# Kernel tuning notes

Hardware: AMD Instinct MI355X
Metric: run time of the kernel (lower is better)

The kernel has to match this reference:

```python
import jax, jax.numpy as jnp
import numpy as np

N_NODES = 50000
HIDDEN = 128
N_EDGES = 1_600_000


def gcn_conv(x, W, b, src, dst, n_nodes):
    """PyG GCNConv: linear, add self-loops, symmetric deg^-1/2 normalization, scatter-sum."""
    h = x @ W  # [N, D]
    # degree with self-loops: 1 + in-degree from edges (edge weight 1)
    deg = jnp.ones((n_nodes,), h.dtype).at[dst].add(1.0)
    dinv = jax.lax.rsqrt(deg)  # deg^{-1/2}, deg >= 1 so no inf
    # neighbor messages: norm_e = dinv[src] * dinv[dst]
    msgs = h[src] * (dinv[src] * dinv[dst])[:, None]  # [E, D]
    agg = jnp.zeros_like(h).at[dst].add(msgs)
    # self-loop contribution: norm = dinv[i]*dinv[i]
    agg = agg + h * (dinv * dinv)[:, None]
    return agg + b


def setup_inputs() -> dict:
    key = jax.random.key(0)
    ks = jax.random.split(key, 7)
    x = jax.random.normal(ks[0], (N_NODES, HIDDEN), dtype=jnp.float32)
    edge_index = jax.random.randint(ks[1], (2, N_EDGES), 0, N_NODES, dtype=jnp.int64)
    s = 1.0 / np.sqrt(HIDDEN)
    W1 = jax.random.uniform(ks[2], (HIDDEN, HIDDEN), jnp.float32, -s, s)
    b1 = jax.random.uniform(ks[3], (HIDDEN,), jnp.float32, -s, s)
    W2 = jax.random.uniform(ks[4], (HIDDEN, HIDDEN), jnp.float32, -s, s)
    b2 = jax.random.uniform(ks[5], (HIDDEN,), jnp.float32, -s, s)
    return {"x": x, "edge_index": edge_index, "W1": W1, "b1": b1, "W2": W2, "b2": b2}


def reference(x, edge_index, W1, b1, W2, b2):
    src, dst = edge_index[0], edge_index[1]
    h = jax.nn.relu(gcn_conv(x, W1, b1, src, dst, N_NODES))
    z = gcn_conv(h, W2, b2, src, dst, N_NODES)
    return z
```

## Files before the change

### kernel.cpp

```cpp
#include <hip/hip_runtime.h>
#include <hip/hip_fp16.h>
#include <type_traits>

#define D 128


__global__ __launch_bounds__(256) void deg_kernel(const int* __restrict__ dst,
                                                  int* __restrict__ deg,
                                                  int* __restrict__ rank, int E) {
  int e = blockIdx.x * 256 + threadIdx.x;
  if (e < E) rank[e] = atomicAdd(&deg[dst[e]], 1);
}


__global__ __launch_bounds__(256) void bsum_kernel(const int* __restrict__ deg,
                                                   int* __restrict__ bsum) {
  __shared__ int ws[4];
  int i0 = blockIdx.x * 1024 + threadIdx.x * 4;
  int4 v = *reinterpret_cast<const int4*>(deg + i0);
  int s = v.x + v.y + v.z + v.w;
  #pragma unroll
  for (int off = 32; off; off >>= 1) s += __shfl_down(s, off);
  if ((threadIdx.x & 63) == 0) ws[threadIdx.x >> 6] = s;
  __syncthreads();
  if (threadIdx.x == 0) bsum[blockIdx.x] = ws[0] + ws[1] + ws[2] + ws[3];
}


__global__ __launch_bounds__(256) void scan_kernel(const int* __restrict__ deg,
                                                   const int* __restrict__ bsum,
                                                   int* __restrict__ offsets,
                                                   float* __restrict__ dinv,
                                                   int N, int E) {
  __shared__ int ts[256];
  int b = blockIdx.x;
  int base = 0;
  for (int t = 0; t < b; ++t) base += bsum[t];

  int i0 = b * 1024 + threadIdx.x * 4;
  int4 v = *reinterpret_cast<const int4*>(deg + i0);
  int t4 = v.x + v.y + v.z + v.w;
  ts[threadIdx.x] = t4;
  __syncthreads();
  #pragma unroll
  for (int off = 1; off < 256; off <<= 1) {
    int u = (threadIdx.x >= off) ? ts[threadIdx.x - off] : 0;
    __syncthreads();
    ts[threadIdx.x] += u;
    __syncthreads();
  }
  int run = base + ts[threadIdx.x] - t4;

  int dd[4] = {v.x, v.y, v.z, v.w};
  #pragma unroll
  for (int k = 0; k < 4; ++k) {
    int i = i0 + k;
    if (i < N) {
      offsets[i] = run;
      dinv[i] = rsqrtf(1.0f + (float)dd[k]);
    }
    run += dd[k];
  }
  if (b == 0 && threadIdx.x == 0) offsets[N] = E;
}


__global__ __launch_bounds__(256) void place_kernel(const int* __restrict__ src,
                                                    const int* __restrict__ dst,
                                                    const int* __restrict__ rank,
                                                    const int* __restrict__ offsets,
                                                    const float* __restrict__ dinv,
                                                    unsigned int* __restrict__ csr, int E) {
  int t = blockIdx.x * 256 + threadIdx.x;
  int e0 = t * 4;
  if (e0 + 4 <= E) {
    int4 s4 = *reinterpret_cast<const int4*>(src + e0);
    int4 d4 = *reinterpret_cast<const int4*>(dst + e0);
    int4 r4 = *reinterpret_cast<const int4*>(rank + e0);
    int ss[4] = {s4.x, s4.y, s4.z, s4.w};
    int dd[4] = {d4.x, d4.y, d4.z, d4.w};
    int rr[4] = {r4.x, r4.y, r4.z, r4.w};
    int pos[4];
    float nm[4];
    #pragma unroll
    for (int k = 0; k < 4; ++k) pos[k] = offsets[dd[k]] + rr[k];
    #pragma unroll
    for (int k = 0; k < 4; ++k) nm[k] = dinv[ss[k]] * dinv[dd[k]];
    #pragma unroll
    for (int k = 0; k < 4; ++k) {
      unsigned int q = (unsigned int)__float2int_rn(nm[k] * 32767.0f);
      csr[pos[k]] = ((unsigned int)ss[k] << 15) | q;
    }
  } else {
    for (int e = e0; e < E; ++e) {
      int s = src[e];
      int d = dst[e];
      int pos = offsets[d] + rank[e];
      float nm = dinv[s] * dinv[d];
      unsigned int q = (unsigned int)__float2int_rn(nm * 32767.0f);
      csr[pos] = ((unsigned int)s << 15) | q;
    }
  }
}


template <typename TI>
__global__ __launch_bounds__(256) void gemm_kernel(const TI* __restrict__ X,
                                                   const float* __restrict__ W,
                                                   __half* __restrict__ H, int N) {
  __shared__ float xs[32 * D];
  int row0 = blockIdx.x * 32;
  if constexpr (std::is_same<TI, float>::value) {
    #pragma unroll
    for (int jj = 0; jj < 4; ++jj) {
      int f4 = threadIdx.x + jj * 256;
      int r = f4 >> 5;
      float4 v = make_float4(0.f, 0.f, 0.f, 0.f);
      if (row0 + r < N) v = *reinterpret_cast<const float4*>(X + (size_t)row0 * D + (size_t)f4 * 4);
      *reinterpret_cast<float4*>(xs + f4 * 4) = v;
    }
  } else {
    #pragma unroll
    for (int jj = 0; jj < 2; ++jj) {
      int g8 = threadIdx.x + jj * 256;
      int r = g8 >> 4;
      uint4 raw = make_uint4(0u, 0u, 0u, 0u);
      if (row0 + r < N)
        raw = *reinterpret_cast<const uint4*>((const __half*)X + (size_t)row0 * D + (size_t)g8 * 8);
      const __half2* hp = reinterpret_cast<const __half2*>(&raw);
      float* dst8 = xs + (size_t)g8 * 8;
      #pragma unroll
      for (int k = 0; k < 4; ++k) {
        float2 f = __half22float2(hp[k]);
        dst8[k * 2] = f.x;
        dst8[k * 2 + 1] = f.y;
      }
    }
  }
  __syncthreads();

  int tx = threadIdx.x & 63;
  int ty = threadIdx.x >> 6;
  int c0 = tx * 2;
  float2 acc[8];
  #pragma unroll
  for (int r = 0; r < 8; ++r) acc[r] = make_float2(0.f, 0.f);
  const float* xbase = xs + ty * 8 * D;

  for (int k = 0; k < D; k += 4) {
    float2 w0 = *reinterpret_cast<const float2*>(W + (size_t)(k + 0) * D + c0);
    float2 w1 = *reinterpret_cast<const float2*>(W + (size_t)(k + 1) * D + c0);
    float2 w2 = *reinterpret_cast<const float2*>(W + (size_t)(k + 2) * D + c0);
    float2 w3 = *reinterpret_cast<const float2*>(W + (size_t)(k + 3) * D + c0);
    #pragma unroll
    for (int r = 0; r < 8; ++r) {
      float4 xv = *reinterpret_cast<const float4*>(xbase + r * D + k);
      acc[r].x = fmaf(xv.x, w0.x, acc[r].x); acc[r].y = fmaf(xv.x, w0.y, acc[r].y);
      acc[r].x = fmaf(xv.y, w1.x, acc[r].x); acc[r].y = fmaf(xv.y, w1.y, acc[r].y);
      acc[r].x = fmaf(xv.z, w2.x, acc[r].x); acc[r].y = fmaf(xv.z, w2.y, acc[r].y);
      acc[r].x = fmaf(xv.w, w3.x, acc[r].x); acc[r].y = fmaf(xv.w, w3.y, acc[r].y);
    }
  }

  #pragma unroll
  for (int r = 0; r < 8; ++r) {
    int row = row0 + ty * 8 + r;
    if (row < N)
      *reinterpret_cast<__half2*>(H + (size_t)row * D + c0) = __floats2half2_rn(acc[r].x, acc[r].y);
  }
}


template <int DO_RELU, typename TO>
__global__ __launch_bounds__(256) void agg_kernel(const __half* __restrict__ H,
                                                  const int* __restrict__ offsets,
                                                  const unsigned int* __restrict__ csr,
                                                  const float* __restrict__ dinv,
                                                  const float* __restrict__ bias,
                                                  TO* __restrict__ out, int N) {
  int n = blockIdx.x * 4 + (threadIdx.x >> 6);
  if (n >= N) return;
  int lane = threadIdx.x & 63;
  int g = lane >> 4;
  int l = lane & 15;

  int beg = offsets[n];
  int end = offsets[n + 1];

  float acc[8];
  #pragma unroll
  for (int k = 0; k < 8; ++k) acc[k] = 0.f;

  const __half* Hl = H + l * 8;

  int j = beg + g;
  for (; j + 12 < end; j += 16) {
    unsigned int p0 = csr[j];
    unsigned int p1 = csr[j + 4];
    unsigned int p2 = csr[j + 8];
    unsigned int p3 = csr[j + 12];
    float m0 = (float)(p0 & 0x7fffu) * (1.0f / 32767.0f);
    float m1 = (float)(p1 & 0x7fffu) * (1.0f / 32767.0f);
    float m2 = (float)(p2 & 0x7fffu) * (1.0f / 32767.0f);
    float m3 = (float)(p3 & 0x7fffu) * (1.0f / 32767.0f);
    uint4 r0 = *reinterpret_cast<const uint4*>(Hl + (size_t)(p0 >> 15) * D);
    uint4 r1 = *reinterpret_cast<const uint4*>(Hl + (size_t)(p1 >> 15) * D);
    uint4 r2 = *reinterpret_cast<const uint4*>(Hl + (size_t)(p2 >> 15) * D);
    uint4 r3 = *reinterpret_cast<const uint4*>(Hl + (size_t)(p3 >> 15) * D);
    const __half2* h0 = reinterpret_cast<const __half2*>(&r0);
    const __half2* h1 = reinterpret_cast<const __half2*>(&r1);
    const __half2* h2 = reinterpret_cast<const __half2*>(&r2);
    const __half2* h3 = reinterpret_cast<const __half2*>(&r3);
    #pragma unroll
    for (int k = 0; k < 4; ++k) {
      float2 f0 = __half22float2(h0[k]);
      float2 f1 = __half22float2(h1[k]);
      float2 f2 = __half22float2(h2[k]);
      float2 f3 = __half22float2(h3[k]);
      acc[2 * k]     = fmaf(f0.x, m0, acc[2 * k]);
      acc[2 * k + 1] = fmaf(f0.y, m0, acc[2 * k + 1]);
      acc[2 * k]     = fmaf(f1.x, m1, acc[2 * k]);
      acc[2 * k + 1] = fmaf(f1.y, m1, acc[2 * k + 1]);
      acc[2 * k]     = fmaf(f2.x, m2, acc[2 * k]);
      acc[2 * k + 1] = fmaf(f2.y, m2, acc[2 * k + 1]);
      acc[2 * k]     = fmaf(f3.x, m3, acc[2 * k]);
      acc[2 * k + 1] = fmaf(f3.y, m3, acc[2 * k + 1]);
    }
  }
  for (; j < end; j += 4) {
    unsigned int p0 = csr[j];
    float m0 = (float)(p0 & 0x7fffu) * (1.0f / 32767.0f);
    uint4 r0 = *reinterpret_cast<const uint4*>(Hl + (size_t)(p0 >> 15) * D);
    const __half2* h0 = reinterpret_cast<const __half2*>(&r0);
    #pragma unroll
    for (int k = 0; k < 4; ++k) {
      float2 f0 = __half22float2(h0[k]);
      acc[2 * k]     = fmaf(f0.x, m0, acc[2 * k]);
      acc[2 * k + 1] = fmaf(f0.y, m0, acc[2 * k + 1]);
    }
  }

  #pragma unroll
  for (int k = 0; k < 8; ++k) {
    acc[k] += __shfl_xor(acc[k], 16);
    acc[k] += __shfl_xor(acc[k], 32);
  }

  if (g == 0) {
    float di = dinv[n];
    float dii = di * di;
    uint4 rs = *reinterpret_cast<const uint4*>(Hl + (size_t)n * D);
    const __half2* hs = reinterpret_cast<const __half2*>(&rs);
    float4 bv0 = *reinterpret_cast<const float4*>(bias + l * 8);
    float4 bv1 = *reinterpret_cast<const float4*>(bias + l * 8 + 4);
    float v[8];
    #pragma unroll
    for (int k = 0; k < 4; ++k) {
      float2 f = __half22float2(hs[k]);
      v[2 * k]     = fmaf(f.x, dii, acc[2 * k]);
      v[2 * k + 1] = fmaf(f.y, dii, acc[2 * k + 1]);
    }
    v[0] += bv0.x; v[1] += bv0.y; v[2] += bv0.z; v[3] += bv0.w;
    v[4] += bv1.x; v[5] += bv1.y; v[6] += bv1.z; v[7] += bv1.w;
    if (DO_RELU) {
      #pragma unroll
      for (int k = 0; k < 8; ++k) v[k] = fmaxf(v[k], 0.f);
    }
    if constexpr (std::is_same<TO, float>::value) {
      float4 o0 = make_float4(v[0], v[1], v[2], v[3]);
      float4 o1 = make_float4(v[4], v[5], v[6], v[7]);
      *reinterpret_cast<float4*>(out + (size_t)n * D + l * 8) = o0;
      *reinterpret_cast<float4*>(out + (size_t)n * D + l * 8 + 4) = o1;
    } else {
      uint4 pk;
      __half2 q0 = __floats2half2_rn(v[0], v[1]);
      __half2 q1 = __floats2half2_rn(v[2], v[3]);
      __half2 q2 = __floats2half2_rn(v[4], v[5]);
      __half2 q3 = __floats2half2_rn(v[6], v[7]);
      pk.x = *reinterpret_cast<unsigned int*>(&q0);
      pk.y = *reinterpret_cast<unsigned int*>(&q1);
      pk.z = *reinterpret_cast<unsigned int*>(&q2);
      pk.w = *reinterpret_cast<unsigned int*>(&q3);
      *reinterpret_cast<uint4*>((__half*)out + (size_t)n * D + l * 8) = pk;
    }
  }
}


extern "C" void kernel_launch(void* const* d_in, const int* in_sizes, int n_in,
                              void* d_out, int out_size, void* d_ws, size_t ws_size,
                              hipStream_t stream) {
  const float* x  = (const float*)d_in[0];
  const int* edge = (const int*)d_in[1];
  const float* W1 = (const float*)d_in[2];
  const float* b1 = (const float*)d_in[3];
  const float* W2 = (const float*)d_in[4];
  const float* b2 = (const float*)d_in[5];
  const int N = in_sizes[0] / D;
  const int E = in_sizes[1] / 2;
  const int* srcp = edge;
  const int* dstp = edge + E;
  float* out = (float*)d_out;

  const int NP = (N + 1023) & ~1023;
  const int SB = NP / 1024;

  auto align = [](size_t v) { return (v + 255) & ~(size_t)255; };
  char* ws = (char*)d_ws;
  size_t o = 0;
  int*   deg     = (int*)(ws + o);             o += align((size_t)NP * 4);
  int*   bsum    = (int*)(ws + o);             o += align((size_t)SB * 4);
  int*   offsets = (int*)(ws + o);             o += align((size_t)(N + 1) * 4);
  int*   rank    = (int*)(ws + o);             o += align((size_t)E * 4);
  float* dinv    = (float*)(ws + o);           o += align((size_t)N * 4);
  unsigned int* csr = (unsigned int*)(ws + o); o += align((size_t)E * 4);
  __half* Hh     = (__half*)(ws + o);          o += align((size_t)N * D * 2);
  __half* h1h    = (__half*)(ws + o);          o += align((size_t)N * D * 2);

  int gemm_blocks = (N + 31) / 32;
  int agg_blocks  = (N + 3) / 4;

  hipMemsetAsync(deg, 0, (size_t)NP * 4, stream);
  deg_kernel<<<(E + 255) / 256, 256, 0, stream>>>(dstp, deg, rank, E);
  bsum_kernel<<<SB, 256, 0, stream>>>(deg, bsum);
  scan_kernel<<<SB, 256, 0, stream>>>(deg, bsum, offsets, dinv, N, E);
  int pl_threads = (E + 3) / 4;
  place_kernel<<<(pl_threads + 255) / 256, 256, 0, stream>>>(srcp, dstp, rank, offsets, dinv, csr, E);

  gemm_kernel<float><<<gemm_blocks, 256, 0, stream>>>(x, W1, Hh, N);
  agg_kernel<1, __half><<<agg_blocks, 256, 0, stream>>>(Hh, offsets, csr, dinv, b1, h1h, N);

  gemm_kernel<__half><<<gemm_blocks, 256, 0, stream>>>(h1h, W2, Hh, N);
  agg_kernel<0, float><<<agg_blocks, 256, 0, stream>>>(Hh, offsets, csr, dinv, b2, out, N);
}
```

Before: 281.3 us.

## Build CSR via per-chunk shared-memory histograms instead of global atomics

Replaces the global atomicAdd degree/rank pass with a two-level counting sort. Edge chunks are histogrammed in LDS per node range, a column-wise prefix over chunks gives per-chunk offsets, and placement uses LDS atomics to assign slots. This removes contended global atomics and the rank array, at the cost of a 128×N count matrix (about 25 MB of extra traffic), re-reading dst once per node-range block, and non-deterministic ordering within chunks.

```diff
diff --git a/kernel.cpp b/kernel.cpp
--- a/kernel.cpp
+++ b/kernel.cpp
@@ -3,13 +3,43 @@
 #include <type_traits>
 
 #define D 128
-
-
-__global__ __launch_bounds__(256) void deg_kernel(const int* __restrict__ dst,
-                                                  int* __restrict__ deg,
-                                                  int* __restrict__ rank, int E) {
-  int e = blockIdx.x * 256 + threadIdx.x;
-  if (e < E) rank[e] = atomicAdd(&deg[dst[e]], 1);
+#define NI 128
+#define NR 25000
+
+
+__global__ __launch_bounds__(1024) void histA_kernel(const int* __restrict__ dst,
+                                                     int* __restrict__ c,
+                                                     int E, int N, int CH) {
+  __shared__ int cnt[NR];
+  int i = blockIdx.x, r = blockIdx.y;
+  int base = r * NR;
+  int kmax = min(NR, N - base);
+  for (int k = threadIdx.x; k < kmax; k += 1024) cnt[k] = 0;
+  __syncthreads();
+  int e0 = i * CH, e1 = min(e0 + CH, E);
+  for (int e = e0 + (int)threadIdx.x; e < e1; e += 1024) {
+    unsigned dr = (unsigned)(dst[e] - base);
+    if (dr < (unsigned)kmax) atomicAdd(&cnt[dr], 1);
+  }
+  __syncthreads();
+  int* ci = c + (size_t)i * N + base;
+  for (int k = threadIdx.x; k < kmax; k += 1024) ci[k] = cnt[k];
+}
+
+
+__global__ __launch_bounds__(256) void histB_kernel(int* __restrict__ c,
+                                                    int* __restrict__ deg, int N) {
+  int n = blockIdx.x * 256 + threadIdx.x;
+  if (n >= N) return;
+  int run = 0;
+  #pragma unroll 8
+  for (int i = 0; i < NI; ++i) {
+    size_t idx = (size_t)i * N + n;
+    int v = c[idx];
+    c[idx] = run;
+    run += v;
+  }
+  deg[n] = run;
 }
 
 
@@ -65,37 +95,27 @@
 }
 
 
-__global__ __launch_bounds__(256) void place_kernel(const int* __restrict__ src,
-                                                    const int* __restrict__ dst,
-                                                    const int* __restrict__ rank,
-                                                    const int* __restrict__ offsets,
-                                                    const float* __restrict__ dinv,
-                                                    unsigned int* __restrict__ csr, int E) {
-  int t = blockIdx.x * 256 + threadIdx.x;
-  int e0 = t * 4;
-  if (e0 + 4 <= E) {
-    int4 s4 = *reinterpret_cast<const int4*>(src + e0);
-    int4 d4 = *reinterpret_cast<const int4*>(dst + e0);
-    int4 r4 = *reinterpret_cast<const int4*>(rank + e0);
-    int ss[4] = {s4.x, s4.y, s4.z, s4.w};
-    int dd[4] = {d4.x, d4.y, d4.z, d4.w};
-    int rr[4] = {r4.x, r4.y, r4.z, r4.w};
-    int pos[4];
-    float nm[4];
-    #pragma unroll
-    for (int k = 0; k < 4; ++k) pos[k] = offsets[dd[k]] + rr[k];
-    #pragma unroll
-    for (int k = 0; k < 4; ++k) nm[k] = dinv[ss[k]] * dinv[dd[k]];
-    #pragma unroll
-    for (int k = 0; k < 4; ++k) {
-      unsigned int q = (unsigned int)__float2int_rn(nm[k] * 32767.0f);
-      csr[pos[k]] = ((unsigned int)ss[k] << 15) | q;
-    }
-  } else {
-    for (int e = e0; e < E; ++e) {
+__global__ __launch_bounds__(1024) void placeC_kernel(const int* __restrict__ src,
+                                                      const int* __restrict__ dst,
+                                                      const int* __restrict__ c,
+                                                      const int* __restrict__ offsets,
+                                                      const float* __restrict__ dinv,
+                                                      unsigned int* __restrict__ csr,
+                                                      int E, int N, int CH) {
+  __shared__ int cnt[NR];
+  int i = blockIdx.x, r = blockIdx.y;
+  int base = r * NR;
+  int kmax = min(NR, N - base);
+  const int* ci = c + (size_t)i * N + base;
+  for (int k = threadIdx.x; k < kmax; k += 1024) cnt[k] = offsets[base + k] + ci[k];
+  __syncthreads();
+  int e0 = i * CH, e1 = min(e0 + CH, E);
+  for (int e = e0 + (int)threadIdx.x; e < e1; e += 1024) {
+    int d = dst[e];
+    unsigned dr = (unsigned)(d - base);
+    if (dr < (unsigned)kmax) {
+      int pos = atomicAdd(&cnt[dr], 1);
       int s = src[e];
-      int d = dst[e];
-      int pos = offsets[d] + rank[e];
       float nm = dinv[s] * dinv[d];
       unsigned int q = (unsigned int)__float2int_rn(nm * 32767.0f);
       csr[pos] = ((unsigned int)s << 15) | q;
@@ -304,6 +324,8 @@
 
   const int NP = (N + 1023) & ~1023;
   const int SB = NP / 1024;
+  const int CH = (E + NI - 1) / NI;
+  const int NRB = (N + NR - 1) / NR;
 
   auto align = [](size_t v) { return (v + 255) & ~(size_t)255; };
   char* ws = (char*)d_ws;
@@ -311,8 +333,8 @@
   int*   deg     = (int*)(ws + o);             o += align((size_t)NP * 4);
   int*   bsum    = (int*)(ws + o);             o += align((size_t)SB * 4);
   int*   offsets = (int*)(ws + o);             o += align((size_t)(N + 1) * 4);
-  int*   rank    = (int*)(ws + o);             o += align((size_t)E * 4);
   float* dinv    = (float*)(ws + o);           o += align((size_t)N * 4);
+  int*   c       = (int*)(ws + o);             o += align((size_t)NI * N * 4);
   unsigned int* csr = (unsigned int*)(ws + o); o += align((size_t)E * 4);
   __half* Hh     = (__half*)(ws + o);          o += align((size_t)N * D * 2);
   __half* h1h    = (__half*)(ws + o);          o += align((size_t)N * D * 2);
@@ -321,11 +343,11 @@
   int agg_blocks  = (N + 3) / 4;
 
   hipMemsetAsync(deg, 0, (size_t)NP * 4, stream);
-  deg_kernel<<<(E + 255) / 256, 256, 0, stream>>>(dstp, deg, rank, E);
+  histA_kernel<<<dim3(NI, NRB), 1024, 0, stream>>>(dstp, c, E, N, CH);
+  histB_kernel<<<(N + 255) / 256, 256, 0, stream>>>(c, deg, N);
   bsum_kernel<<<SB, 256, 0, stream>>>(deg, bsum);
   scan_kernel<<<SB, 256, 0, stream>>>(deg, bsum, offsets, dinv, N, E);
-  int pl_threads = (E + 3) / 4;
-  place_kernel<<<(pl_threads + 255) / 256, 256, 0, stream>>>(srcp, dstp, rank, offsets, dinv, csr, E);
+  placeC_kernel<<<dim3(NI, NRB), 1024, 0, stream>>>(srcp, dstp, c, offsets, dinv, csr, E, N, CH);
 
   gemm_kernel<float><<<gemm_blocks, 256, 0, stream>>>(x, W1, Hh, N);
   agg_kernel<1, __half><<<agg_blocks, 256, 0, stream>>>(Hh, offsets, csr, dinv, b1, h1h, N);
```

New measurement: 241.2 us. 1.17x faster.
